# Performance work log

Measured on AMD Instinct MI355X. Metric: run time of the kernel, lower is better.

Reference implementation:

```python
import jax, jax.numpy as jnp
import numpy as np

DOWNSAMPLE = 1

def _meshgrid(oh, ow):
    # grid rows: x in [-1,1] repeated per row, y in [-1,1] per column, ones -> [3, oh*ow]
    x_t = jnp.tile(jnp.linspace(-1.0, 1.0, ow, dtype=jnp.float32)[None, :], (oh, 1))
    y_t = jnp.tile(jnp.linspace(-1.0, 1.0, oh, dtype=jnp.float32)[:, None], (1, ow))
    ones = jnp.ones((1, oh * ow), dtype=jnp.float32)
    return jnp.concatenate([x_t.reshape(1, -1), y_t.reshape(1, -1), ones], axis=0)

def setup_inputs() -> dict:
    key = jax.random.key(0)
    k1, k2 = jax.random.split(key)
    B, C, H, W = 32, 16, 256, 256
    inp = jax.random.normal(k1, (B, C, H, W), dtype=jnp.float32)
    # theta near identity with noise so sampling is non-degenerate
    ident = jnp.array([1.0, 0.0, 0.0, 0.0, 1.0, 0.0], dtype=jnp.float32)
    theta = ident[None, :] + 0.1 * jax.random.normal(k2, (B, 6), dtype=jnp.float32)
    return {"input": inp, "theta": theta}

def reference(input, theta):
    B, C, H, W = input.shape
    oh, ow = H // DOWNSAMPLE, W // DOWNSAMPLE
    grid = _meshgrid(oh, ow)                      # [3, N] with N = oh*ow
    Tg = jnp.einsum('bij,jn->bin', theta.reshape(B, 2, 3), grid)  # [B,2,N]
    x = jnp.clip(Tg[:, 0], -1.0, 1.0)             # [B,N]
    y = jnp.clip(Tg[:, 1], -1.0, 1.0)
    x = (x + 1.0) * 0.5 * (W - 1)
    y = (y + 1.0) * 0.5 * (H - 1)
    x0f = jnp.floor(x); y0f = jnp.floor(y)
    x1f = x0f + 1.0;    y1f = y0f + 1.0
    x0 = x0f.astype(jnp.int32); y0 = y0f.astype(jnp.int32)
    x1 = jnp.minimum(x1f, W - 1).astype(jnp.int32)
    y1 = jnp.minimum(y1f, H - 1).astype(jnp.int32)
    im = jnp.transpose(input, (0, 2, 3, 1))        # [B,H,W,C] channels-last like the original
    b = jnp.arange(B, dtype=jnp.int32)[:, None]    # [B,1] broadcast over N
    Ia = im[b, y0, x0]                             # [B,N,C] four irregular gathers
    Ib = im[b, y1, x0]
    Ic = im[b, y0, x1]
    Id = im[b, y1, x1]
    wa = ((x1f - x) * (y1f - y))[..., None]
    wb = ((x1f - x) * (y - y0f))[..., None]
    wc = ((x - x0f) * (y1f - y))[..., None]
    wd = ((x - x0f) * (y - y0f))[..., None]
    out = wa * Ia + wb * Ib + wc * Ic + wd * Id    # [B,N,C]
    out = out.reshape(B, oh, ow, C)
    return jnp.transpose(out, (0, 3, 1, 2))        # [B,C,oh,ow]
```

## Files before the change

kernel.cpp:

```cpp
#include <hip/hip_runtime.h>

#define BB 32
#define CC 16
#define HH 256
#define WW 256
#define HWSZ (HH * WW)
#define ROWS 2
#define NBLK (BB * HH / ROWS)
#define NXCD 8

typedef float f2 __attribute__((ext_vector_type(2)));

__global__ __launch_bounds__(256) void st_bilinear_pair_kernel(
    const float* __restrict__ input,
    const float* __restrict__ theta,
    float* __restrict__ out)
{
    int bid = blockIdx.x;
    int wg = (bid & (NXCD - 1)) * (NBLK / NXCD) + (bid >> 3);

    int b  = wg >> 7;
    int ty = wg & 127;
    int oy = ty * ROWS + (threadIdx.x >> 7);
    int ox0 = (threadIdx.x & 127) * 2;

    const float* th = theta + b * 6;
    float t0 = th[0], t1 = th[1], t2 = th[2];
    float t3 = th[3], t4 = th[4], t5 = th[5];

    const float step = 2.0f / 255.0f;
    float gy = -1.0f + oy * step;
    float cx = t1 * gy + t2;
    float cy = t4 * gy + t5;

    int   off[2];
    float w00[2], w01[2], w10[2], w11[2];

    #pragma unroll
    for (int i = 0; i < 2; ++i) {
        float gx = -1.0f + (ox0 + i) * step;
        float xs = fminf(fmaxf(t0 * gx + cx, -1.0f), 1.0f);
        float ys = fminf(fmaxf(t3 * gx + cy, -1.0f), 1.0f);
        float x = (xs + 1.0f) * 127.5f;
        float y = (ys + 1.0f) * 127.5f;

        float bxf = fminf(floorf(x), 254.0f);
        float byf = fminf(floorf(y), 254.0f);
        float fx = x - bxf;
        float fy = y - byf;

        off[i] = (int)byf * WW + (int)bxf;
        w00[i] = (1.0f - fx) * (1.0f - fy);
        w01[i] = fx * (1.0f - fy);
        w10[i] = (1.0f - fx) * fy;
        w11[i] = fx * fy;
    }

    const float* ibase = input + (size_t)b * CC * HWSZ;
    float* obase = out + (size_t)b * CC * HWSZ + oy * WW + ox0;

    #pragma unroll 4
    for (int c = 0; c < CC; ++c) {
        const float* p = ibase + c * HWSZ;

        f2 a0, a1, b0, b1;
        __builtin_memcpy(&a0, p + off[0], 8);
        __builtin_memcpy(&a1, p + off[0] + WW, 8);
        __builtin_memcpy(&b0, p + off[1], 8);
        __builtin_memcpy(&b1, p + off[1] + WW, 8);

        float o0 = a0.x * w00[0] + a0.y * w01[0] + a1.x * w10[0] + a1.y * w11[0];
        float o1 = b0.x * w00[1] + b0.y * w01[1] + b1.x * w10[1] + b1.y * w11[1];

        f2 ov; ov.x = o0; ov.y = o1;
        __builtin_nontemporal_store(ov, (f2*)(obase + c * HWSZ));
    }
}

extern "C" void kernel_launch(void* const* d_in, const int* in_sizes, int n_in,
                              void* d_out, int out_size, void* d_ws, size_t ws_size,
                              hipStream_t stream) {
    const float* input = (const float*)d_in[0];
    const float* theta = (const float*)d_in[1];
    float* out = (float*)d_out;

    dim3 block(256);
    dim3 grid(NBLK);
    hipLaunchKernelGGL(st_bilinear_pair_kernel, grid, block, 0, stream,
                       input, theta, out);
}
```

Before: 54.84 us.

## Stage per-tile input footprint in LDS and gather bilinear taps from shared memory

Switches from row-pair blocks to 64x16 output tiles. Each block computes the bounding box of the transformed tile, cooperatively loads that input window per channel into a 56x96 LDS buffer with float4 loads, then reads the four bilinear taps from LDS, falling back to global memory for pixels outside the window. Each thread now produces four outputs and writes them with a float4 nontemporal store. The goal is coalesced global reads and reuse of neighbouring pixels across threads. The cost is two __syncthreads per channel, channel loads that are no longer overlapped, and some redundant loading of halo rows.

```diff
diff --git a/kernel.cpp b/kernel.cpp
--- a/kernel.cpp
+++ b/kernel.cpp
@@ -5,75 +5,140 @@
 #define HH 256
 #define WW 256
 #define HWSZ (HH * WW)
-#define ROWS 2
-#define NBLK (BB * HH / ROWS)
+
+#define TW 64
+#define TH 16
+#define XT (WW / TW)
+#define YT (HH / TH)
+#define NBLK (BB * XT * YT)
 #define NXCD 8
 
+#define SROWS 56
+#define SCOLS 96
+#define SF4 (SCOLS / 4)
+
 typedef float f2 __attribute__((ext_vector_type(2)));
+typedef float f4 __attribute__((ext_vector_type(4)));
 
-__global__ __launch_bounds__(256) void st_bilinear_pair_kernel(
+__global__ __launch_bounds__(256) void st_lds_kernel(
     const float* __restrict__ input,
     const float* __restrict__ theta,
     float* __restrict__ out)
 {
+    __shared__ float S[SROWS * SCOLS];
+
     int bid = blockIdx.x;
     int wg = (bid & (NXCD - 1)) * (NBLK / NXCD) + (bid >> 3);
 
-    int b  = wg >> 7;
-    int ty = wg & 127;
-    int oy = ty * ROWS + (threadIdx.x >> 7);
-    int ox0 = (threadIdx.x & 127) * 2;
+    int b  = wg >> 6;
+    int r  = wg & 63;
+    int yt = r >> 2;
+    int xt = r & 3;
+
+    int tid = threadIdx.x;
+    int qy = tid >> 4;
+    int qx = tid & 15;
+    int oy  = yt * TH + qy;
+    int oxb = xt * TW + qx * 4;
 
     const float* th = theta + b * 6;
     float t0 = th[0], t1 = th[1], t2 = th[2];
     float t3 = th[3], t4 = th[4], t5 = th[5];
 
     const float step = 2.0f / 255.0f;
+
+    float gxa = -1.0f + (xt * TW) * step;
+    float gxb = -1.0f + (xt * TW + TW - 1) * step;
+    float gya = -1.0f + (yt * TH) * step;
+    float gyb = -1.0f + (yt * TH + TH - 1) * step;
+
+    float x00 = t0 * gxa + t1 * gya + t2, x01 = t0 * gxa + t1 * gyb + t2;
+    float x10 = t0 * gxb + t1 * gya + t2, x11 = t0 * gxb + t1 * gyb + t2;
+    float y00 = t3 * gxa + t4 * gya + t5, y01 = t3 * gxa + t4 * gyb + t5;
+    float y10 = t3 * gxb + t4 * gya + t5, y11 = t3 * gxb + t4 * gyb + t5;
+
+    float xmn = fminf(fminf(x00, x01), fminf(x10, x11));
+    float xmx = fmaxf(fmaxf(x00, x01), fmaxf(x10, x11));
+    float ymn = fminf(fminf(y00, y01), fminf(y10, y11));
+    float ymx = fmaxf(fmaxf(y00, y01), fmaxf(y10, y11));
+    xmn = fminf(fmaxf(xmn, -1.0f), 1.0f) ;
+    xmx = fminf(fmaxf(xmx, -1.0f), 1.0f);
+    ymn = fminf(fmaxf(ymn, -1.0f), 1.0f);
+    ymx = fminf(fmaxf(ymx, -1.0f), 1.0f);
+    float pxmn = (xmn + 1.0f) * 127.5f, pxmx = (xmx + 1.0f) * 127.5f;
+    float pymn = (ymn + 1.0f) * 127.5f, pymx = (ymx + 1.0f) * 127.5f;
+
+    int cx0 = (int)floorf(pxmn) - 2;
+    cx0 = max(0, min(cx0, WW - SCOLS)) & ~3;
+    int ry0 = (int)floorf(pymn) - 2;
+    ry0 = max(0, min(ry0, HH - 1));
+    int ryend = min((int)floorf(pymx) + 3, HH - 1);
+    int rows = min(min(ryend - ry0 + 1, SROWS), HH - ry0);
+    int nf4 = rows * SF4;
+
+    int   off[4], goff[4];
+    float w00[4], w01[4], w10[4], w11[4];
+    bool  ok[4];
     float gy = -1.0f + oy * step;
-    float cx = t1 * gy + t2;
-    float cy = t4 * gy + t5;
-
-    int   off[2];
-    float w00[2], w01[2], w10[2], w11[2];
+    float cxp = t1 * gy + t2;
+    float cyp = t4 * gy + t5;
 
     #pragma unroll
-    for (int i = 0; i < 2; ++i) {
-        float gx = -1.0f + (ox0 + i) * step;
-        float xs = fminf(fmaxf(t0 * gx + cx, -1.0f), 1.0f);
-        float ys = fminf(fmaxf(t3 * gx + cy, -1.0f), 1.0f);
+    for (int j = 0; j < 4; ++j) {
+        float gx = -1.0f + (oxb + j) * step;
+        float xs = fminf(fmaxf(t0 * gx + cxp, -1.0f), 1.0f);
+        float ys = fminf(fmaxf(t3 * gx + cyp, -1.0f), 1.0f);
         float x = (xs + 1.0f) * 127.5f;
         float y = (ys + 1.0f) * 127.5f;
-
         float bxf = fminf(floorf(x), 254.0f);
         float byf = fminf(floorf(y), 254.0f);
-        float fx = x - bxf;
-        float fy = y - byf;
+        float fx = x - bxf, fy = y - byf;
+        int bx = (int)bxf, by = (int)byf;
 
-        off[i] = (int)byf * WW + (int)bxf;
-        w00[i] = (1.0f - fx) * (1.0f - fy);
-        w01[i] = fx * (1.0f - fy);
-        w10[i] = (1.0f - fx) * fy;
-        w11[i] = fx * fy;
+        w00[j] = (1.0f - fx) * (1.0f - fy);
+        w01[j] = fx * (1.0f - fy);
+        w10[j] = (1.0f - fx) * fy;
+        w11[j] = fx * fy;
+
+        int lx = bx - cx0, ly = by - ry0;
+        ok[j] = (lx >= 0) && (lx <= SCOLS - 2) && (ly >= 0) && (ly <= rows - 2);
+        off[j]  = ly * SCOLS + lx;
+        goff[j] = by * WW + bx;
     }
 
     const float* ibase = input + (size_t)b * CC * HWSZ;
-    float* obase = out + (size_t)b * CC * HWSZ + oy * WW + ox0;
+    float* obase = out + (size_t)b * CC * HWSZ + (size_t)oy * WW + oxb;
 
-    #pragma unroll 4
     for (int c = 0; c < CC; ++c) {
+        __syncthreads();
+        const float* src = ibase + c * HWSZ + ry0 * WW + cx0;
+        for (int idx = tid; idx < nf4; idx += 256) {
+            int rr = (idx * 2731) >> 16;
+            int cq = idx - rr * SF4;
+            f4 v = *(const f4*)(src + rr * WW + cq * 4);
+            *(f4*)&S[rr * SCOLS + cq * 4] = v;
+        }
+        __syncthreads();
+
         const float* p = ibase + c * HWSZ;
-
-        f2 a0, a1, b0, b1;
-        __builtin_memcpy(&a0, p + off[0], 8);
-        __builtin_memcpy(&a1, p + off[0] + WW, 8);
-        __builtin_memcpy(&b0, p + off[1], 8);
-        __builtin_memcpy(&b1, p + off[1] + WW, 8);
-
-        float o0 = a0.x * w00[0] + a0.y * w01[0] + a1.x * w10[0] + a1.y * w11[0];
-        float o1 = b0.x * w00[1] + b0.y * w01[1] + b1.x * w10[1] + b1.y * w11[1];
-
-        f2 ov; ov.x = o0; ov.y = o1;
-        __builtin_nontemporal_store(ov, (f2*)(obase + c * HWSZ));
+        f4 ov;
+        #pragma unroll
+        for (int j = 0; j < 4; ++j) {
+            float v00, v01, v10, v11;
+            if (ok[j]) {
+                v00 = S[off[j]];
+                v01 = S[off[j] + 1];
+                v10 = S[off[j] + SCOLS];
+                v11 = S[off[j] + SCOLS + 1];
+            } else {
+                f2 a, bb;
+                __builtin_memcpy(&a,  p + goff[j], 8);
+                __builtin_memcpy(&bb, p + goff[j] + WW, 8);
+                v00 = a.x; v01 = a.y; v10 = bb.x; v11 = bb.y;
+            }
+            ov[j] = v00 * w00[j] + v01 * w01[j] + v10 * w10[j] + v11 * w11[j];
+        }
+        __builtin_nontemporal_store(ov, (f4*)(obase + c * HWSZ));
     }
 }
 
@@ -86,6 +151,6 @@
 
     dim3 block(256);
     dim3 grid(NBLK);
-    hipLaunchKernelGGL(st_bilinear_pair_kernel, grid, block, 0, stream,
+    hipLaunchKernelGGL(st_lds_kernel, grid, block, 0, stream,
                        input, theta, out);
 }
```

Result: slower. 57.30 us (+4.5%).
